# Kernel optimization log

Measured on AMD Instinct MI355X. Metric: run time of the kernel, lower is better.

## Reference

```python
import jax, jax.numpy as jnp
import numpy as np
from jax import lax

B, T = 64, 1000
DEC, ENC, ATT, FILT, KS = 1024, 512, 128, 32, 31
PAD = (KS - 1) // 2


def setup_inputs() -> dict:
    key = jax.random.key(0)
    ks = jax.random.split(key, 9)
    return {
        "decoder_hidden": jax.random.normal(ks[0], (B, DEC), dtype=jnp.float32),
        "encoder_outputs": jax.random.normal(ks[1], (B, T, ENC), dtype=jnp.float32),
        "prev_weights": jax.random.uniform(ks[2], (B, T), dtype=jnp.float32),
        "prev_weights_cum": jax.random.uniform(ks[3], (B, T), dtype=jnp.float32),
        "mask": jnp.zeros((B, T), dtype=bool),
        # learned parameters (torch Linear weight layout: [out, in])
        "conv_w": jax.random.normal(ks[4], (FILT, 2, KS), dtype=jnp.float32) * 0.05,
        "loc_proj_w": jax.random.normal(ks[5], (ATT, FILT), dtype=jnp.float32) * 0.05,
        "query_w": jax.random.normal(ks[6], (ATT, DEC), dtype=jnp.float32) * 0.02,
        "key_w": jax.random.normal(ks[7], (ATT, ENC), dtype=jnp.float32) * 0.02,
        "value_w": jax.random.normal(ks[8], (1, ATT), dtype=jnp.float32) * 0.05,
    }


def reference(decoder_hidden, encoder_outputs, prev_weights, prev_weights_cum,
              mask, conv_w, loc_proj_w, query_w, key_w, value_w):
    # query: (B, ATT)
    query = decoder_hidden @ query_w.T
    # keys: (B, T, ATT)
    keys = jnp.einsum('bte,ae->bta', encoder_outputs, key_w)
    # location features: (B, 2, T) -> conv -> (B, FILT, T)
    loc_feats = jnp.stack([prev_weights, prev_weights_cum], axis=1)
    proc_loc = lax.conv_general_dilated(
        loc_feats, conv_w, window_strides=(1,), padding=[(PAD, PAD)],
        dimension_numbers=('NCH', 'OIH', 'NCH'))
    # (B, T, FILT) -> (B, T, ATT)
    proc_loc = jnp.einsum('bft,af->bta', proc_loc, loc_proj_w)
    # energies: (B, T)
    hidden = jnp.tanh(query[:, None, :] + keys + proc_loc)
    energies = jnp.einsum('bta,a->bt', hidden, value_w[0])
    energies = jnp.where(mask, -jnp.inf, energies)
    attention_weights = jax.nn.softmax(energies, axis=1)
    # context: (B, ENC)
    context = jnp.einsum('bt,bte->be', attention_weights, encoder_outputs)
    return context, attention_weights
```

## Files before the change

### kernel.cpp

```cpp
#include <hip/hip_runtime.h>
#include <hip/hip_bf16.h>
#include <math.h>

#define BB   64
#define TT   1000
#define DEC  1024
#define ENCD 512
#define ATT  128
#define FILT 32
#define KSZ  31
#define PADW 15
#define BT   64
#define KC   64
#define XWN  96

typedef __attribute__((ext_vector_type(8))) short bf16x8;
typedef __attribute__((ext_vector_type(4))) float f32x4;

static __device__ __forceinline__ ushort f2bf(float f) {
    union { float f; unsigned u; } v; v.f = f;
    unsigned r = (v.u + 0x7FFFu + ((v.u >> 16) & 1u)) >> 16;
    return (ushort)r;
}

static __device__ __forceinline__ bf16x8 cvt8(float4 lo, float4 hi) {
    union { __hip_bfloat162 h[4]; bf16x8 v; } u;
    u.h[0] = __float22bfloat162_rn(make_float2(lo.x, lo.y));
    u.h[1] = __float22bfloat162_rn(make_float2(lo.z, lo.w));
    u.h[2] = __float22bfloat162_rn(make_float2(hi.x, hi.y));
    u.h[3] = __float22bfloat162_rn(make_float2(hi.z, hi.w));
    return u.v;
}

static __device__ __forceinline__ float fast_tanh(float x) {
    float e = __expf(2.f * x);
    return 1.f - 2.f * __builtin_amdgcn_rcpf(e + 1.f);
}

static __device__ __forceinline__ void gl2lds16(const void* g, void* l) {
    __builtin_amdgcn_global_load_lds(
        (const __attribute__((address_space(1))) unsigned*)g,
        (__attribute__((address_space(3))) unsigned*)l, 16, 0, 0);
}

__global__ __launch_bounds__(256) void k_prep(const float* __restrict__ kw,
                                              const float* __restrict__ cw,
                                              const float* __restrict__ lpw,
                                              const float* __restrict__ dh,
                                              const float* __restrict__ qw,
                                              const float* __restrict__ vw,
                                              ushort* __restrict__ kwbF,
                                              float* __restrict__ q,
                                              float* __restrict__ Mbuf) {
    __shared__ float qred[128];
    if (blockIdx.x < 32) {
        int idx = blockIdx.x * 256 + threadIdx.x;
        int l  = idx & 63;
        int n  = (idx >> 6) & 7;
        int ks = (idx >> 9) & 1;
        int c  = idx >> 10;
        int a  = n * 16 + (l & 15);
        int k0 = c * 64 + ks * 32 + (l >> 4) * 8;
        ushort u[8];
        #pragma unroll
        for (int j = 0; j < 8; ++j) u[j] = f2bf(kw[a * ENCD + k0 + j]);
        *(uint4*)&kwbF[(size_t)idx * 8] = *(const uint4*)u;
    } else if (blockIdx.x < 36) {
        int idx = (blockIdx.x - 32) * 256 + threadIdx.x;
        int l  = idx & 63;
        int n  = (idx >> 6) & 7;
        int ks = (idx >> 9) & 1;
        int a  = n * 16 + (l & 15);
        int s  = l >> 4;
        ushort u[8];
        #pragma unroll
        for (int j = 0; j < 8; ++j) {
            int k = s * 8 + j;
            float v = 0.f;
            if (k < KSZ) {
                #pragma unroll
                for (int f = 0; f < FILT; ++f)
                    v += cw[(f * 2 + ks) * KSZ + k] * lpw[a * FILT + f];
            }
            u[j] = f2bf(v);
        }
        *(uint4*)&kwbF[(size_t)(((16 + ks) * 8 + n) * 64 + l) * 8] = *(const uint4*)u;
    } else if (blockIdx.x == 36) {
        if (threadIdx.x < 64) {
            float m0 = fabsf(vw[threadIdx.x]) + fabsf(vw[threadIdx.x + 64]);
            #pragma unroll
            for (int off = 1; off < 64; off <<= 1) m0 += __shfl_xor(m0, off, 64);
            if (threadIdx.x == 0) Mbuf[0] = m0;
        }
    } else {
        int b  = blockIdx.x - 37;
        int a  = threadIdx.x & 127;
        int kh = threadIdx.x >> 7;
        const float* dhb = dh + b * DEC + kh * 512;
        const float* qwa = qw + a * DEC + kh * 512;
        float s = 0.f;
        #pragma unroll 4
        for (int k = 0; k < 512; k += 4) {
            float4 x = *(const float4*)&dhb[k];
            float4 w = *(const float4*)&qwa[k];
            s += x.x * w.x + x.y * w.y + x.z * w.z + x.w * w.w;
        }
        if (kh == 1) qred[a] = s;
        __syncthreads();
        if (kh == 0) q[b * ATT + a] = s + qred[a];
    }
}

__global__ __launch_bounds__(256) void k_energies(
    const float* __restrict__ enc, const float* __restrict__ pw,
    const float* __restrict__ pwc, const unsigned char* __restrict__ mask,
    const ushort* __restrict__ kwbF, const float* __restrict__ vw,
    const float* __restrict__ q, const float* __restrict__ Mbuf,
    float* __restrict__ expE, float* __restrict__ pctx,
    float* __restrict__ ps)
{
    __shared__ __align__(16) float Ab[2][BT * 64];
    __shared__ __align__(16) float xw[2][XWN];
    __shared__ float pehalf[2][BT];
    __shared__ float sExp[BT];

    const int b    = blockIdx.x;
    const int tile = blockIdx.y;
    const int t0   = tile * BT;
    const int tid  = threadIdx.x;
    const int w    = tid >> 6;
    const int l    = tid & 63;
    const int r    = l & 15;
    const int sl   = l >> 4;
    const int wt   = w & 1;
    const int wa   = w >> 1;

    const float* encb = enc + (size_t)b * TT * ENCD;

    const int c4src = (l & 15) ^ (w * 4 + (l >> 4));
    const float* aSrc[4];
    #pragma unroll
    for (int j = 0; j < 4; ++j) {
        int rw  = (j * 4 + w) * 4 + (l >> 4);
        int tg  = t0 + rw; if (tg >= TT) tg = TT - 1;
        aSrc[j] = encb + (size_t)tg * ENCD + c4src * 4;
    }

    for (int i = tid; i < 2 * XWN; i += 256) {
        int c  = i / XWN;
        int ii = i - c * XWN;
        int tg = t0 + ii - PADW;
        const float* src = c ? pwc : pw;
        xw[c][ii] = (ii < BT + KSZ - 1 && tg >= 0 && tg < TT) ? src[b * TT + tg] : 0.f;
    }

    uint4 bfr0[2][4], bfr1[2][4];
    auto loadB = [&](uint4 (&dst)[2][4], int c) {
        #pragma unroll
        for (int ks = 0; ks < 2; ++ks)
            #pragma unroll
            for (int nn = 0; nn < 4; ++nn)
                dst[ks][nn] = *(const uint4*)&kwbF[(size_t)(((c * 2 + ks) * 8 + wa * 4 + nn) * 64 + l) * 8];
    };
    auto issueA = [&](int c, int buf) {
        #pragma unroll
        for (int j = 0; j < 4; ++j)
            gl2lds16(aSrc[j] + c * KC, (char*)Ab[buf] + (j * 4 + w) * 1024);
    };

    f32x4 acc[2][4];
    #pragma unroll
    for (int i = 0; i < 2; ++i)
        #pragma unroll
        for (int n = 0; n < 4; ++n) acc[i][n] = (f32x4){0.f, 0.f, 0.f, 0.f};

    auto compute = [&](int c, const uint4 (&bfr)[2][4]) {
        #pragma unroll
        for (int ks = 0; ks < 2; ++ks) {
            const int s2 = 2 * (ks * 4 + sl);
            bf16x8 af[2];
            #pragma unroll
            for (int i = 0; i < 2; ++i) {
                int row = wt * 32 + i * 16 + r;
                if (c < 8) {
                    const char* base = (const char*)Ab[c & 1] + row * 256;
                    float4 alo = *(const float4*)(base + ((s2 ^ r) << 4));
                    float4 ahi = *(const float4*)(base + (((s2 | 1) ^ r) << 4));
                    af[i] = cvt8(alo, ahi);
                } else {
                    const float* xp = &xw[ks][row + sl * 8];
                    float4 alo = make_float4(xp[0], xp[1], xp[2], xp[3]);
                    float4 ahi = make_float4(xp[4], xp[5], xp[6], xp[7]);
                    af[i] = cvt8(alo, ahi);
                }
            }
            __builtin_amdgcn_s_setprio(1);
            #pragma unroll
            for (int i = 0; i < 2; ++i)
                #pragma unroll
                for (int nn = 0; nn < 4; ++nn)
                    acc[i][nn] = __builtin_amdgcn_mfma_f32_16x16x32_bf16(
                        af[i], *(const bf16x8*)&bfr[ks][nn], acc[i][nn], 0, 0, 0);
            __builtin_amdgcn_s_setprio(0);
        }
    };

    issueA(0, 0); loadB(bfr0, 0);
    issueA(1, 1); loadB(bfr1, 1);
    asm volatile("s_waitcnt vmcnt(12) lgkmcnt(0)" ::: "memory");
    __builtin_amdgcn_sched_barrier(0);
    __builtin_amdgcn_s_barrier();

    #pragma unroll
    for (int c = 0; c < 9; ++c) {
        if (c & 1) compute(c, bfr1); else compute(c, bfr0);
        if (c == 8) break;
        __builtin_amdgcn_s_barrier();
        __builtin_amdgcn_sched_barrier(0);
        if (c + 2 <= 8) {
            if (c + 2 <= 7) issueA(c + 2, c & 1);
            if (c & 1) loadB(bfr1, c + 2); else loadB(bfr0, c + 2);
        }
        if (c <= 5)      asm volatile("s_waitcnt vmcnt(12)" ::: "memory");
        else if (c == 6) asm volatile("s_waitcnt vmcnt(8)"  ::: "memory");
        else             asm volatile("s_waitcnt vmcnt(0)"  ::: "memory");
        __builtin_amdgcn_sched_barrier(0);
        __builtin_amdgcn_s_barrier();
    }

    const float* qb = q + b * ATT;
    const float M = Mbuf[0];
    float pe[2][4];
    #pragma unroll
    for (int i = 0; i < 2; ++i)
        #pragma unroll
        for (int rr = 0; rr < 4; ++rr) pe[i][rr] = 0.f;
    #pragma unroll
    for (int nn = 0; nn < 4; ++nn) {
        int a = wa * 64 + nn * 16 + r;
        float vvn = vw[a];
        float qvn = qb[a];
        #pragma unroll
        for (int i = 0; i < 2; ++i)
            #pragma unroll
            for (int rr = 0; rr < 4; ++rr)
                pe[i][rr] += vvn * fast_tanh(acc[i][nn][rr] + qvn);
    }
    #pragma unroll
    for (int m = 1; m < 16; m <<= 1)
        #pragma unroll
        for (int i = 0; i < 2; ++i)
            #pragma unroll
            for (int rr = 0; rr < 4; ++rr)
                pe[i][rr] += __shfl_xor(pe[i][rr], m, 64);
    if (r == 0) {
        #pragma unroll
        for (int i = 0; i < 2; ++i)
            #pragma unroll
            for (int rr = 0; rr < 4; ++rr)
                pehalf[wa][wt * 32 + i * 16 + sl * 4 + rr] = pe[i][rr];
    }
    __syncthreads();
    if (tid < BT) {
        int t = t0 + tid;
        float e = pehalf[0][tid] + pehalf[1][tid];
        float v = 0.f;
        if (t < TT && !mask[b * TT + t]) v = __expf(e - M);
        if (t < TT) expE[b * TT + t] = v;
        sExp[tid] = v;
        float sv = v;
        #pragma unroll
        for (int off = 1; off < 64; off <<= 1) sv += __shfl_xor(sv, off, 64);
        if (tid == 0) ps[b * 16 + tile] = sv;
    }
    __syncthreads();

    const int tmax = (TT - t0 < BT) ? (TT - t0) : BT;
    float2 cacc = make_float2(0.f, 0.f);
    const float* pbase = encb + (size_t)t0 * ENCD + tid * 2;
    for (int t = 0; t < tmax; ++t) {
        float s = sExp[t];
        float2 v = *(const float2*)(pbase + (size_t)t * ENCD);
        cacc.x += s * v.x; cacc.y += s * v.y;
    }
    *(float2*)&pctx[(size_t)(b * 16 + tile) * ENCD + tid * 2] = cacc;
}

__global__ __launch_bounds__(256) void k_ctx_reduce(const float* __restrict__ pctx,
                                                    const float* __restrict__ ps,
                                                    const float* __restrict__ expE,
                                                    float* __restrict__ ctx,
                                                    float* __restrict__ wout) {
    int bid = blockIdx.x, tid = threadIdx.x;
    __shared__ float sps[16];
    int b = (bid < BB) ? bid : (bid - BB);
    if (tid < 16) sps[tid] = ps[b * 16 + tid];
    __syncthreads();
    float s = 0.f;
    #pragma unroll
    for (int i = 0; i < 16; ++i) s += sps[i];
    float inv = 1.f / s;
    if (bid < BB) {
        float2 a = make_float2(0.f, 0.f);
        #pragma unroll
        for (int i = 0; i < 16; ++i) {
            float2 v = *(const float2*)&pctx[(size_t)(b * 16 + i) * ENCD + tid * 2];
            a.x += v.x; a.y += v.y;
        }
        a.x *= inv; a.y *= inv;
        *(float2*)&ctx[b * ENCD + tid * 2] = a;
    } else {
        for (int t = tid; t < TT; t += 256)
            wout[b * TT + t] = expE[b * TT + t] * inv;
    }
}

extern "C" void kernel_launch(void* const* d_in, const int* in_sizes, int n_in,
                              void* d_out, int out_size, void* d_ws, size_t ws_size,
                              hipStream_t stream) {
    const float* dh   = (const float*)d_in[0];
    const float* enc  = (const float*)d_in[1];
    const float* pw   = (const float*)d_in[2];
    const float* pwc  = (const float*)d_in[3];
    const unsigned char* mask = (const unsigned char*)d_in[4];
    const float* cw   = (const float*)d_in[5];
    const float* lpw  = (const float*)d_in[6];
    const float* qw   = (const float*)d_in[7];
    const float* kw   = (const float*)d_in[8];
    const float* vw   = (const float*)d_in[9];

    float* out_ctx = (float*)d_out;
    float* out_w   = out_ctx + BB * ENCD;

    float* wsf    = (float*)d_ws;
    float*  q     = wsf;
    float*  expE  = wsf + 8192;
    float*  ps    = wsf + 8192 + 64000;
    float*  pctx  = wsf + 8192 + 64000 + 1024;
    ushort* kwbF  = (ushort*)(wsf + 8192 + 64000 + 1024 + 524288);
    float*  Mbuf  = wsf + 8192 + 64000 + 1024 + 524288 + 36864;

    k_prep    <<<dim3(101),    dim3(256), 0, stream>>>(kw, cw, lpw, dh, qw, vw, kwbF, q, Mbuf);
    k_energies<<<dim3(BB, 16), dim3(256), 0, stream>>>(enc, pw, pwc, mask, kwbF, vw, q, Mbuf, expE, pctx, ps);
    k_ctx_reduce <<<dim3(128), dim3(256), 0, stream>>>(pctx, ps, expE, out_ctx, out_w);
}
```

Before: 67.52 us.

## Stage full encoder tile in LDS and reuse it for the context reduction

The energies kernel now uses 32-row time tiles (32 tiles per batch) and loads the whole 32x512 fp32 encoder tile into a 64KB LDS buffer in two halves, replacing the double-buffered 64-wide K chunk pipeline. Each wave now owns 32 attention columns instead of splitting by time and attention halves. The weighted context sum reads the encoder rows back from LDS rather than re-reading them from global memory, removing the second pass over encoder_outputs. The cost is large LDS use per block, which limits occupancy, plus twice as many partial context rows to reduce in the final kernel.

```diff
diff --git a/kernel.cpp b/kernel.cpp
--- a/kernel.cpp
+++ b/kernel.cpp
@@ -10,9 +10,9 @@
 #define FILT 32
 #define KSZ  31
 #define PADW 15
-#define BT   64
-#define KC   64
-#define XWN  96
+#define BT   32
+#define NTL  32
+#define XWN  64
 
 typedef __attribute__((ext_vector_type(8))) short bf16x8;
 typedef __attribute__((ext_vector_type(4))) float f32x4;
@@ -119,9 +119,9 @@
     float* __restrict__ expE, float* __restrict__ pctx,
     float* __restrict__ ps)
 {
-    __shared__ __align__(16) float Ab[2][BT * 64];
+    __shared__ __align__(16) float As[BT * ENCD];
     __shared__ __align__(16) float xw[2][XWN];
-    __shared__ float pehalf[2][BT];
+    __shared__ float pequad[4][BT];
     __shared__ float sExp[BT];
 
     const int b    = blockIdx.x;
@@ -132,19 +132,8 @@
     const int l    = tid & 63;
     const int r    = l & 15;
     const int sl   = l >> 4;
-    const int wt   = w & 1;
-    const int wa   = w >> 1;
 
     const float* encb = enc + (size_t)b * TT * ENCD;
-
-    const int c4src = (l & 15) ^ (w * 4 + (l >> 4));
-    const float* aSrc[4];
-    #pragma unroll
-    for (int j = 0; j < 4; ++j) {
-        int rw  = (j * 4 + w) * 4 + (l >> 4);
-        int tg  = t0 + rw; if (tg >= TT) tg = TT - 1;
-        aSrc[j] = encb + (size_t)tg * ENCD + c4src * 4;
-    }
 
     for (int i = tid; i < 2 * XWN; i += 256) {
         int c  = i / XWN;
@@ -153,80 +142,100 @@
         const float* src = c ? pwc : pw;
         xw[c][ii] = (ii < BT + KSZ - 1 && tg >= 0 && tg < TT) ? src[b * TT + tg] : 0.f;
     }
-
-    uint4 bfr0[2][4], bfr1[2][4];
-    auto loadB = [&](uint4 (&dst)[2][4], int c) {
+    __builtin_amdgcn_sched_barrier(0);
+
+    #pragma unroll
+    for (int j = 0; j < 8; ++j) {
+        int rl = w * 8 + j;
+        int rg = t0 + rl; if (rg >= TT) rg = TT - 1;
+        const float* src = encb + (size_t)rg * ENCD + (size_t)(sl * 16 + (r ^ (rl & 15))) * 4;
+        gl2lds16(src, (char*)As + rl * 2048);
+    }
+    __builtin_amdgcn_sched_barrier(0);
+
+    uint4 bA[2][2], bB[2][2], bC[2][2], bD[2][2], bW[2][2];
+    auto loadB = [&](uint4 (&dst)[2][2], int c) {
         #pragma unroll
         for (int ks = 0; ks < 2; ++ks)
             #pragma unroll
-            for (int nn = 0; nn < 4; ++nn)
-                dst[ks][nn] = *(const uint4*)&kwbF[(size_t)(((c * 2 + ks) * 8 + wa * 4 + nn) * 64 + l) * 8];
+            for (int nn = 0; nn < 2; ++nn)
+                dst[ks][nn] = *(const uint4*)&kwbF[(size_t)(((c * 2 + ks) * 8 + w * 2 + nn) * 64 + l) * 8];
     };
-    auto issueA = [&](int c, int buf) {
-        #pragma unroll
-        for (int j = 0; j < 4; ++j)
-            gl2lds16(aSrc[j] + c * KC, (char*)Ab[buf] + (j * 4 + w) * 1024);
-    };
-
-    f32x4 acc[2][4];
+    loadB(bA, 0); loadB(bB, 1); loadB(bC, 2); loadB(bD, 3); loadB(bW, 8);
+    __builtin_amdgcn_sched_barrier(0);
+
+    #pragma unroll
+    for (int j = 0; j < 8; ++j) {
+        int rl = w * 8 + j;
+        int rg = t0 + rl; if (rg >= TT) rg = TT - 1;
+        const float* src = encb + (size_t)rg * ENCD + 256 + (size_t)(sl * 16 + (r ^ (rl & 15))) * 4;
+        gl2lds16(src, (char*)As + rl * 2048 + 1024);
+    }
+    __builtin_amdgcn_sched_barrier(0);
+    asm volatile("s_waitcnt vmcnt(8) lgkmcnt(0)" ::: "memory");
+    __builtin_amdgcn_sched_barrier(0);
+    __builtin_amdgcn_s_barrier();
+
+    f32x4 acc[2][2];
     #pragma unroll
     for (int i = 0; i < 2; ++i)
         #pragma unroll
-        for (int n = 0; n < 4; ++n) acc[i][n] = (f32x4){0.f, 0.f, 0.f, 0.f};
-
-    auto compute = [&](int c, const uint4 (&bfr)[2][4]) {
+        for (int n = 0; n < 2; ++n) acc[i][n] = (f32x4){0.f, 0.f, 0.f, 0.f};
+
+    auto compute = [&](int c, const uint4 (&bfr)[2][2]) {
         #pragma unroll
         for (int ks = 0; ks < 2; ++ks) {
-            const int s2 = 2 * (ks * 4 + sl);
+            const int u = ks * 8 + sl * 2;
             bf16x8 af[2];
             #pragma unroll
             for (int i = 0; i < 2; ++i) {
-                int row = wt * 32 + i * 16 + r;
-                if (c < 8) {
-                    const char* base = (const char*)Ab[c & 1] + row * 256;
-                    float4 alo = *(const float4*)(base + ((s2 ^ r) << 4));
-                    float4 ahi = *(const float4*)(base + (((s2 | 1) ^ r) << 4));
-                    af[i] = cvt8(alo, ahi);
-                } else {
-                    const float* xp = &xw[ks][row + sl * 8];
-                    float4 alo = make_float4(xp[0], xp[1], xp[2], xp[3]);
-                    float4 ahi = make_float4(xp[4], xp[5], xp[6], xp[7]);
-                    af[i] = cvt8(alo, ahi);
-                }
+                int row = i * 16 + r;
+                const char* base = (const char*)As + row * 2048 + c * 256;
+                float4 alo = *(const float4*)(base + ((u ^ (row & 15)) << 4));
+                float4 ahi = *(const float4*)(base + (((u + 1) ^ (row & 15)) << 4));
+                af[i] = cvt8(alo, ahi);
             }
             __builtin_amdgcn_s_setprio(1);
             #pragma unroll
             for (int i = 0; i < 2; ++i)
                 #pragma unroll
-                for (int nn = 0; nn < 4; ++nn)
+                for (int nn = 0; nn < 2; ++nn)
                     acc[i][nn] = __builtin_amdgcn_mfma_f32_16x16x32_bf16(
                         af[i], *(const bf16x8*)&bfr[ks][nn], acc[i][nn], 0, 0, 0);
             __builtin_amdgcn_s_setprio(0);
         }
     };
-
-    issueA(0, 0); loadB(bfr0, 0);
-    issueA(1, 1); loadB(bfr1, 1);
-    asm volatile("s_waitcnt vmcnt(12) lgkmcnt(0)" ::: "memory");
+    auto computeFeat = [&](const uint4 (&bfr)[2][2]) {
+        #pragma unroll
+        for (int ks = 0; ks < 2; ++ks) {
+            bf16x8 af[2];
+            #pragma unroll
+            for (int i = 0; i < 2; ++i) {
+                int row = i * 16 + r;
+                const float* xp = &xw[ks][row + sl * 8];
+                af[i] = cvt8(make_float4(xp[0], xp[1], xp[2], xp[3]),
+                             make_float4(xp[4], xp[5], xp[6], xp[7]));
+            }
+            __builtin_amdgcn_s_setprio(1);
+            #pragma unroll
+            for (int i = 0; i < 2; ++i)
+                #pragma unroll
+                for (int nn = 0; nn < 2; ++nn)
+                    acc[i][nn] = __builtin_amdgcn_mfma_f32_16x16x32_bf16(
+                        af[i], *(const bf16x8*)&bfr[ks][nn], acc[i][nn], 0, 0, 0);
+            __builtin_amdgcn_s_setprio(0);
+        }
+    };
+
+    compute(0, bA); compute(1, bB); compute(2, bC); compute(3, bD);
+    computeFeat(bW);
+
+    asm volatile("s_waitcnt vmcnt(0)" ::: "memory");
     __builtin_amdgcn_sched_barrier(0);
     __builtin_amdgcn_s_barrier();
 
-    #pragma unroll
-    for (int c = 0; c < 9; ++c) {
-        if (c & 1) compute(c, bfr1); else compute(c, bfr0);
-        if (c == 8) break;
-        __builtin_amdgcn_s_barrier();
-        __builtin_amdgcn_sched_barrier(0);
-        if (c + 2 <= 8) {
-            if (c + 2 <= 7) issueA(c + 2, c & 1);
-            if (c & 1) loadB(bfr1, c + 2); else loadB(bfr0, c + 2);
-        }
-        if (c <= 5)      asm volatile("s_waitcnt vmcnt(12)" ::: "memory");
-        else if (c == 6) asm volatile("s_waitcnt vmcnt(8)"  ::: "memory");
-        else             asm volatile("s_waitcnt vmcnt(0)"  ::: "memory");
-        __builtin_amdgcn_sched_barrier(0);
-        __builtin_amdgcn_s_barrier();
-    }
+    loadB(bA, 4); loadB(bB, 5); loadB(bC, 6); loadB(bD, 7);
+    compute(4, bA); compute(5, bB); compute(6, bC); compute(7, bD);
 
     const float* qb = q + b * ATT;
     const float M = Mbuf[0];
@@ -236,8 +245,8 @@
         #pragma unroll
         for (int rr = 0; rr < 4; ++rr) pe[i][rr] = 0.f;
     #pragma unroll
-    for (int nn = 0; nn < 4; ++nn) {
-        int a = wa * 64 + nn * 16 + r;
+    for (int nn = 0; nn < 2; ++nn) {
+        int a = w * 32 + nn * 16 + r;
         float vvn = vw[a];
         float qvn = qb[a];
         #pragma unroll
@@ -258,32 +267,36 @@
         for (int i = 0; i < 2; ++i)
             #pragma unroll
             for (int rr = 0; rr < 4; ++rr)
-                pehalf[wa][wt * 32 + i * 16 + sl * 4 + rr] = pe[i][rr];
+                pequad[w][i * 16 + sl * 4 + rr] = pe[i][rr];
     }
     __syncthreads();
     if (tid < BT) {
         int t = t0 + tid;
-        float e = pehalf[0][tid] + pehalf[1][tid];
+        float e = pequad[0][tid] + pequad[1][tid] + pequad[2][tid] + pequad[3][tid];
         float v = 0.f;
         if (t < TT && !mask[b * TT + t]) v = __expf(e - M);
         if (t < TT) expE[b * TT + t] = v;
         sExp[tid] = v;
         float sv = v;
         #pragma unroll
-        for (int off = 1; off < 64; off <<= 1) sv += __shfl_xor(sv, off, 64);
-        if (tid == 0) ps[b * 16 + tile] = sv;
+        for (int off = 1; off < 32; off <<= 1) sv += __shfl_xor(sv, off, 64);
+        if (tid == 0) ps[b * NTL + tile] = sv;
     }
     __syncthreads();
 
-    const int tmax = (TT - t0 < BT) ? (TT - t0) : BT;
-    float2 cacc = make_float2(0.f, 0.f);
-    const float* pbase = encb + (size_t)t0 * ENCD + tid * 2;
-    for (int t = 0; t < tmax; ++t) {
-        float s = sExp[t];
-        float2 v = *(const float2*)(pbase + (size_t)t * ENCD);
-        cacc.x += s * v.x; cacc.y += s * v.y;
-    }
-    *(float2*)&pctx[(size_t)(b * 16 + tile) * ENCD + tid * 2] = cacc;
+    {
+        const int U   = tid >> 1;
+        const int sub = (tid & 1) * 8;
+        float2 cacc = make_float2(0.f, 0.f);
+        #pragma unroll 4
+        for (int t = 0; t < BT; ++t) {
+            float s = sExp[t];
+            int byte = t * 2048 + (((U & ~15) | ((U ^ (t & 15)) & 15)) << 4) + sub;
+            float2 v = *(const float2*)((const char*)As + byte);
+            cacc.x += s * v.x; cacc.y += s * v.y;
+        }
+        *(float2*)&pctx[(size_t)(b * NTL + tile) * ENCD + tid * 2] = cacc;
+    }
 }
 
 __global__ __launch_bounds__(256) void k_ctx_reduce(const float* __restrict__ pctx,
@@ -292,19 +305,19 @@
                                                     float* __restrict__ ctx,
                                                     float* __restrict__ wout) {
     int bid = blockIdx.x, tid = threadIdx.x;
-    __shared__ float sps[16];
+    __shared__ float sps[NTL];
     int b = (bid < BB) ? bid : (bid - BB);
-    if (tid < 16) sps[tid] = ps[b * 16 + tid];
+    if (tid < NTL) sps[tid] = ps[b * NTL + tid];
     __syncthreads();
     float s = 0.f;
     #pragma unroll
-    for (int i = 0; i < 16; ++i) s += sps[i];
+    for (int i = 0; i < NTL; ++i) s += sps[i];
     float inv = 1.f / s;
     if (bid < BB) {
         float2 a = make_float2(0.f, 0.f);
         #pragma unroll
-        for (int i = 0; i < 16; ++i) {
-            float2 v = *(const float2*)&pctx[(size_t)(b * 16 + i) * ENCD + tid * 2];
+        for (int i = 0; i < NTL; ++i) {
+            float2 v = *(const float2*)&pctx[(size_t)(b * NTL + i) * ENCD + tid * 2];
             a.x += v.x; a.y += v.y;
         }
         a.x *= inv; a.y *= inv;
@@ -336,11 +349,11 @@
     float*  q     = wsf;
     float*  expE  = wsf + 8192;
     float*  ps    = wsf + 8192 + 64000;
-    float*  pctx  = wsf + 8192 + 64000 + 1024;
-    ushort* kwbF  = (ushort*)(wsf + 8192 + 64000 + 1024 + 524288);
-    float*  Mbuf  = wsf + 8192 + 64000 + 1024 + 524288 + 36864;
-
-    k_prep    <<<dim3(101),    dim3(256), 0, stream>>>(kw, cw, lpw, dh, qw, vw, kwbF, q, Mbuf);
-    k_energies<<<dim3(BB, 16), dim3(256), 0, stream>>>(enc, pw, pwc, mask, kwbF, vw, q, Mbuf, expE, pctx, ps);
-    k_ctx_reduce <<<dim3(128), dim3(256), 0, stream>>>(pctx, ps, expE, out_ctx, out_w);
-}
+    float*  pctx  = wsf + 8192 + 64000 + 2048;
+    ushort* kwbF  = (ushort*)(wsf + 8192 + 64000 + 2048 + 1048576);
+    float*  Mbuf  = wsf + 8192 + 64000 + 2048 + 1048576 + 36864;
+
+    k_prep    <<<dim3(101),     dim3(256), 0, stream>>>(kw, cw, lpw, dh, qw, vw, kwbF, q, Mbuf);
+    k_energies<<<dim3(BB, NTL), dim3(256), 0, stream>>>(enc, pw, pwc, mask, kwbF, vw, q, Mbuf, expE, pctx, ps);
+    k_ctx_reduce <<<dim3(128),  dim3(256), 0, stream>>>(pctx, ps, expE, out_ctx, out_w);
+}
```

Measured after the change: 63.90 us (median of 3 runs). 5.4% less time.
